# Performance work log

Hardware: AMD Instinct MI355X
Metric: run time of the kernel (lower is better)

The kernel has to match this reference:

```python
import jax, jax.numpy as jnp
import numpy as np

H = 488          # hardcoded grid size in the module
K = 6            # n_targets
ITERS = 10       # n_iterations
RADIUS = 2       # sample_radius (int, used in slicing)
RECLEN = 2 * RADIUS + 1   # avgpool kernel in TorchModalitySampler (upscale=1)
RES = 0.25
THR = 3.0 / RES  # mask threshold on distances


def _greedy_sample(hm):
    """TorchModalitySampler greedy peak extraction for one [H,H] heatmap."""
    aw = H - RECLEN + 1  # avgpool output size (stride 1, valid)

    def step(hm, _):
        # avgpool(kernel=RECLEN, stride=1)
        agg = jax.lax.reduce_window(hm, 0.0, jax.lax.add,
                                    (RECLEN, RECLEN), (1, 1), 'VALID') / (RECLEN * RECLEN)
        flat = jnp.argmax(agg)              # first occurrence of max (row-major)
        r, c = flat // aw, flat % aw
        win = jax.lax.dynamic_slice(hm, (r, c), (RECLEN, RECLEN))
        max_val = win.max()
        # torch.nonzero(hm == max_val)[0] == first row-major match
        fh = jnp.argmax(hm == max_val)
        pt = jnp.stack([fh // H, fh % H]).astype(jnp.float32)
        conf = win.sum()
        hm = jax.lax.dynamic_update_slice(hm, jnp.zeros((RECLEN, RECLEN), hm.dtype), (r, c))
        return hm, (pt, conf)

    _, (pts, confs) = jax.lax.scan(step, hm, None, length=K)
    return pts, confs  # [K,2] float, [K] float


def setup_inputs() -> dict:
    key = jax.random.key(0)
    heatmap = jax.random.uniform(key, (32, 1, H, H), dtype=jnp.float32)
    return {"heatmap": heatmap}


def reference(heatmap):
    B = heatmap.shape[0]
    hm2d = heatmap[:, 0]                       # [B,H,H]
    clusters, _pre_conf = jax.vmap(_greedy_sample)(hm2d)   # [B,K,2]

    ii, jj = jnp.meshgrid(jnp.arange(H), jnp.arange(H), indexing='ij')
    indices = jnp.stack([ii, jj], -1).reshape(-1, 2).astype(jnp.float32)  # [N,2]
    hm_flat = hm2d.reshape(B, -1)              # [B,N]

    def body(_, cl):
        # d: [B,K,N] distances from each cluster to every pixel
        d = jnp.maximum(jnp.linalg.norm(indices[None, None] - cl[:, :, None], axis=-1), 0.001)
        m = d.min(axis=1)                      # [B,N] nearest-cluster distance
        w = (d < THR) * (hm_flat[:, None] / d) * (m[:, None] / d)  # [B,K,N]
        return jnp.einsum('bkn,nd->bkd', w, indices) / w.sum(-1, keepdims=True)

    clusters = jax.lax.fori_loop(0, ITERS, body, clusters)
    new_clusters = jnp.round(clusters).astype(jnp.int32)   # [B,K,2]

    def conf_one(hm, c):
        win = jax.lax.dynamic_slice(hm, (c[0] - RADIUS, c[1] - RADIUS), (2 * RADIUS, 2 * RADIUS))
        return win.sum()

    confidences = jax.vmap(lambda hm, cs: jax.vmap(lambda c: conf_one(hm, c))(cs))(hm2d, new_clusters)
    return new_clusters, confidences
```

## Files before the change

### kernel.cpp

```cpp
#include <hip/hip_runtime.h>

#define H   488
#define HH  (H*H)
#define AW  484
#define KK  6
#define BB  32
#define NB4 (HH/4)

#define SCALE 8388608.0f

#define PHYS(j) ((j) + ((j) >> 5))
#define HPAD 504

__device__ __forceinline__ float mload(const float* h, int i, int j,
                                       const int* rr, const int* rc, int nr) {
    float v = h[i * H + j];
    for (int t = 0; t < nr; ++t)
        if ((unsigned)(i - rr[t]) < 5u && (unsigned)(j - rc[t]) < 5u) v = 0.0f;
    return v;
}

__device__ __forceinline__ unsigned long long mkkey(int s, int c) {
    return ((unsigned long long)(unsigned)s << 32) | (unsigned)~(unsigned)c;
}

__global__ __launch_bounds__(512) void kA(const float* __restrict__ hm,
                                          unsigned long long* __restrict__ blockK) {
    int b  = blockIdx.x & 31;
    int g  = blockIdx.x >> 5;
    int r0 = g * 8;
    int nw = (r0 + 8 <= AW) ? 8 : (AW - r0);
    const float* h = hm + b * HH;
    __shared__ int colsum[8][HPAD];

    int j = threadIdx.x;
    if (j < H) {
        int v[12];
        #pragma unroll
        for (int i = 0; i < 12; ++i) {
            int row = r0 + i;
            v[i] = (row < H) ? (int)(h[row * H + j] * SCALE) : 0;
        }
        int pj = PHYS(j);
        #pragma unroll
        for (int w = 0; w < 8; ++w)
            colsum[w][pj] = v[w] + v[w + 1] + v[w + 2] + v[w + 3] + v[w + 4];
    }
    __syncthreads();

    int wave = threadIdx.x >> 6, lane = threadIdx.x & 63;
    if (wave < nw) {
        int r = r0 + wave;
        int c0 = lane * 8;
        int cs[13];
        #pragma unroll
        for (int t = 0; t < 13; ++t) {
            int idx = c0 + t;
            cs[t] = (idx < H) ? colsum[wave][PHYS(idx)] : 0;
        }
        int s = cs[0] + cs[1] + cs[2] + cs[3] + cs[4];
        unsigned long long best = (c0 < AW) ? mkkey(s, c0) : 0ull;
        #pragma unroll
        for (int t = 1; t < 8; ++t) {
            s += cs[t + 4] - cs[t - 1];
            int c = c0 + t;
            unsigned long long k2 = (c < AW) ? mkkey(s, c) : 0ull;
            if (k2 > best) best = k2;
        }
        #pragma unroll
        for (int off = 4; off; off >>= 1) {
            unsigned long long o = __shfl_down(best, (unsigned)off);
            if (o > best) best = o;
        }
        if ((lane & 7) == 0) {
            int p = lane >> 3;
            blockK[(b * 8 + p) * AW + r] = best;
        }
    }
}

__global__ __launch_bounds__(640) void kB(const float* __restrict__ hm,
                                          const unsigned long long* __restrict__ blockK,
                                          int* __restrict__ rectR, int* __restrict__ rectC,
                                          float* __restrict__ maxv, int* __restrict__ scanres) {
    int b = blockIdx.x;
    const float* h = hm + b * HH;
    __shared__ unsigned long long bK[8 * AW];
    __shared__ unsigned long long rvK[AW];
    __shared__ int rrS[KK], rcS[KK];
    __shared__ int selRs, selCs;
    int tid = threadIdx.x, wave = tid >> 6, lane = tid & 63;

    if (tid < AW) {
        unsigned long long kk[8];
        #pragma unroll
        for (int p = 0; p < 8; ++p) kk[p] = blockK[(b * 8 + p) * AW + tid];
        unsigned long long mk = kk[0];
        #pragma unroll
        for (int p = 1; p < 8; ++p) if (kk[p] > mk) mk = kk[p];
        #pragma unroll
        for (int p = 0; p < 8; ++p) bK[p * AW + tid] = kk[p];
        rvK[tid] = ((mk >> 32) << 20) | ((unsigned long long)(1023 - tid) << 10) | (mk & 0x3FF);
    }
    __syncthreads();

    unsigned long long partK = 0ull;
    int prlo = 0, prhi = -1;

    for (int step = 0; step < KK; ++step) {
        if (wave == 0) {
            unsigned long long win = 0ull;
            if (step == 0) {
                #pragma unroll
                for (int t = 0; t < 8; ++t) {
                    int idx = t * 64 + lane;
                    if (idx < AW) { unsigned long long v = rvK[idx]; if (v > win) win = v; }
                }
                #pragma unroll
                for (int off = 32; off; off >>= 1) {
                    unsigned long long o = __shfl_down(win, (unsigned)off);
                    if (o > win) win = o;
                }
            } else {
                if (lane <= prhi - prlo) win = rvK[prlo + lane];
                if (lane == 9) { if (partK > win) win = partK; }
                #pragma unroll
                for (int off = 8; off; off >>= 1) {
                    unsigned long long o = __shfl_down(win, (unsigned)off);
                    if (o > win) win = o;
                }
            }
            if (lane == 0) {
                int C = 1023 - (int)(win & 0x3FF);
                int R = 1023 - (int)((win >> 10) & 0x3FF);
                rrS[step] = R; rcS[step] = C;
                selRs = R; selCs = C;
            }
        } else if (wave == 1 && step > 0) {
            int m = step - 1;
            int R1 = rrS[m], C1 = rcS[m];
            float wv = -1.0f;
            if (lane < 25) wv = mload(h, R1 + lane / 5, C1 + lane % 5, rrS, rcS, m);
            #pragma unroll
            for (int off = 32; off; off >>= 1) wv = fmaxf(wv, __shfl_down(wv, (unsigned)off));
            if (lane == 0) {
                maxv[b * KK + m]    = wv;
                rectR[b * KK + m]   = R1;
                rectC[b * KK + m]   = C1;
                scanres[b * KK + m] = 0x7fffffff;
            }
        }
        __syncthreads();
        if (step == KK - 1) break;

        int R = selRs, C = selCs;
        int rlo = R > 4 ? R - 4 : 0, rhi = R + 4 < AW ? R + 4 : AW - 1;
        int nr = rhi - rlo + 1;
        if (wave >= 1 && wave <= nr) {
            int r = rlo + (wave - 1);
            int cb0 = (C > 4 ? C - 4 : 0) >> 6;
            int cb1 = ((C + 4 < AW ? C + 4 : AW - 1)) >> 6;
            bool two = (cb1 > cb0);
            int rrL[KK], rcL[KK];
            #pragma unroll
            for (int t = 0; t < KK; ++t) { rrL[t] = rrS[t]; rcL[t] = rcS[t]; }
            int jA0 = cb0 * 64 + lane, jB0 = jA0 + 64;
            int jA1 = cb1 * 64 + lane, jB1 = jA1 + 64;
            float vA0[5], vB0[5], vA1[5], vB1[5];
            #pragma unroll
            for (int i = 0; i < 5; ++i) {
                vA0[i] = (jA0 < H) ? h[(r + i) * H + jA0] : 0.0f;
                vB0[i] = (lane < 4 && jB0 < H) ? h[(r + i) * H + jB0] : 0.0f;
                vA1[i] = (two && jA1 < H) ? h[(r + i) * H + jA1] : 0.0f;
                vB1[i] = (two && lane < 4 && jB1 < H) ? h[(r + i) * H + jB1] : 0.0f;
            }
            #pragma unroll
            for (int t = 0; t < KK; ++t) if (t <= step) {
                int rt = rrL[t], ct = rcL[t];
                #pragma unroll
                for (int i = 0; i < 5; ++i) {
                    if ((unsigned)(r + i - rt) < 5u) {
                        if ((unsigned)(jA0 - ct) < 5u) vA0[i] = 0.0f;
                        if ((unsigned)(jB0 - ct) < 5u) vB0[i] = 0.0f;
                        if ((unsigned)(jA1 - ct) < 5u) vA1[i] = 0.0f;
                        if ((unsigned)(jB1 - ct) < 5u) vB1[i] = 0.0f;
                    }
                }
            }
            int csA0 = 0, csB0 = 0, csA1 = 0, csB1 = 0;
            #pragma unroll
            for (int i = 0; i < 5; ++i) {
                csA0 += (int)(vA0[i] * SCALE); csB0 += (int)(vB0[i] * SCALE);
                csA1 += (int)(vA1[i] * SCALE); csB1 += (int)(vB1[i] * SCALE);
            }
            int s0 = 0, s1 = 0;
            #pragma unroll
            for (int k = 0; k < 5; ++k) {
                int a0 = __shfl_down(csA0, (unsigned)k);
                int a1 = __shfl_down(csA1, (unsigned)k);
                int srcb = lane + k - 64; if (srcb < 0) srcb = 0;
                int b0v = __shfl(csB0, srcb);
                int b1v = __shfl(csB1, srcb);
                s0 += (lane + k < 64) ? a0 : b0v;
                s1 += (lane + k < 64) ? a1 : b1v;
            }
            int c0col = cb0 * 64 + lane, c1col = cb1 * 64 + lane;
            unsigned long long kA_ = (c0col < AW) ? mkkey(s0, c0col) : 0ull;
            unsigned long long kB_ = (two && c1col < AW) ? mkkey(s1, c1col) : 0ull;
            #pragma unroll
            for (int off = 32; off; off >>= 1) {
                unsigned long long oA = __shfl_down(kA_, (unsigned)off);
                unsigned long long oB = __shfl_down(kB_, (unsigned)off);
                if (oA > kA_) kA_ = oA;
                if (oB > kB_) kB_ = oB;
            }
            unsigned long long keyA = __shfl(kA_, 0);
            unsigned long long keyB = __shfl(kB_, 0);
            unsigned long long cand = (lane < 8) ? bK[lane * AW + r] : 0ull;
            if (lane == cb0) cand = keyA;
            if (two && lane == cb1) cand = keyB;
            #pragma unroll
            for (int off = 4; off; off >>= 1) {
                unsigned long long o = __shfl_down(cand, (unsigned)off);
                if (o > cand) cand = o;
            }
            if (lane == 0) {
                rvK[r] = ((cand >> 32) << 20) | ((unsigned long long)(1023 - r) << 10) | (cand & 0x3FF);
                bK[cb0 * AW + r] = keyA;
                if (two) bK[cb1 * AW + r] = keyB;
            }
        } else if (wave == 0) {
            unsigned long long c0 = 0ull;
            #pragma unroll
            for (int t = 0; t < 8; ++t) {
                int idx = t * 64 + lane;
                if (idx < AW && (idx < rlo || idx > rhi)) {
                    unsigned long long v = rvK[idx];
                    if (v > c0) c0 = v;
                }
            }
            #pragma unroll
            for (int off = 32; off; off >>= 1) {
                unsigned long long o = __shfl_down(c0, (unsigned)off);
                if (o > c0) c0 = o;
            }
            partK = __shfl(c0, 0);
            prlo = rlo; prhi = rhi;
        }
        __syncthreads();
    }
    if (wave == 1) {
        int m = KK - 1;
        int R1 = rrS[m], C1 = rcS[m];
        float wv = -1.0f;
        if (lane < 25) wv = mload(h, R1 + lane / 5, C1 + lane % 5, rrS, rcS, m);
        #pragma unroll
        for (int off = 32; off; off >>= 1) wv = fmaxf(wv, __shfl_down(wv, (unsigned)off));
        if (lane == 0) {
            maxv[b * KK + m]    = wv;
            rectR[b * KK + m]   = R1;
            rectC[b * KK + m]   = C1;
            scanres[b * KK + m] = 0x7fffffff;
        }
    }
}

__global__ __launch_bounds__(256) void kC(const float* __restrict__ hm,
                                          const int* __restrict__ rectR, const int* __restrict__ rectC,
                                          const float* __restrict__ maxv, int* __restrict__ scanres) {
    int b     = blockIdx.x & 31;
    int chunk = blockIdx.x >> 5;
    float mv[KK];
    int rr[5], rc[5], lim[KK];
    #pragma unroll
    for (int s = 0; s < KK; ++s) mv[s] = maxv[b * KK + s];
    float minmv = mv[0];
    #pragma unroll
    for (int s = 1; s < KK; ++s) minmv = fminf(minmv, mv[s]);
    #pragma unroll
    for (int t = 0; t < 5; ++t) { rr[t] = rectR[b * KK + t]; rc[t] = rectC[b * KK + t]; }
    int limmax = 0;
    #pragma unroll
    for (int s = 0; s < KK; ++s) {
        lim[s] = (rectR[b * KK + s] + 4) * H + rectC[b * KK + s] + 4;
        limmax = lim[s] > limmax ? lim[s] : limmax;
    }
    const float4* h4 = (const float4*)(hm + b * HH);
    int local[KK];
    #pragma unroll
    for (int s = 0; s < KK; ++s) local[s] = 0x7fffffff;
    for (int i4 = chunk * 256 + threadIdx.x; i4 < NB4; i4 += 8192) {
        if (4 * i4 > limmax) break;
        float4 v = h4[i4];
        float m4 = fmaxf(fmaxf(v.x, v.y), fmaxf(v.z, v.w));
        if (m4 >= minmv) {
            float vs[4] = {v.x, v.y, v.z, v.w};
            #pragma unroll
            for (int e = 0; e < 4; ++e) {
                #pragma unroll
                for (int s = 0; s < KK; ++s) {
                    if (vs[e] == mv[s]) {
                        int n = 4 * i4 + e;
                        if (n <= lim[s]) {
                            int i = n / H, j = n - i * H;
                            bool masked = false;
                            for (int t = 0; t < s; ++t)
                                if ((unsigned)(i - rr[t]) < 5u && (unsigned)(j - rc[t]) < 5u) masked = true;
                            if (!masked && n < local[s]) local[s] = n;
                        }
                    }
                }
            }
        }
    }
    __shared__ int sm[KK];
    if (threadIdx.x < KK) sm[threadIdx.x] = 0x7fffffff;
    __syncthreads();
    #pragma unroll
    for (int s = 0; s < KK; ++s)
        if (local[s] != 0x7fffffff) atomicMin(&sm[s], local[s]);
    __syncthreads();
    if (threadIdx.x < KK && sm[threadIdx.x] != 0x7fffffff)
        atomicMin(&scanres[b * KK + threadIdx.x], sm[threadIdx.x]);
}

__global__ __launch_bounds__(768) void kD(const float* __restrict__ hm,
                                          const int* __restrict__ scanres, float* __restrict__ out) {
    int b = blockIdx.x;
    const float* h = hm + b * HH;
    __shared__ float cly[2][KK], clx[2][KK];
    __shared__ float part[KK][2][3];
    int tid = threadIdx.x;
    if (tid < KK) {
        int fh = scanres[b * KK + tid];
        cly[0][tid] = (float)(fh / H);
        clx[0][tid] = (float)(fh % H);
    }
    __syncthreads();
    int wave = tid >> 6, lane = tid & 63;
    int k = wave >> 1, half = wave & 1;
    int base = half * 64 + lane;

    int di_[4], dj_[4]; bool act_[4];
    #pragma unroll
    for (int s = 0; s < 4; ++s) { act_[s] = false; di_[s] = 0; dj_[s] = 0; }
    {
        int pos = 0;
        #pragma unroll
        for (int r = 0; r < 24; ++r) {
            const int di = r - 11;
            const int u = (di > 0) ? (di - 1) : -di;
            const int vt[12] = {11, 11, 11, 11, 11, 10, 10, 9, 8, 7, 6, 4};
            const int vl = vt[u];
            const int cnt = 2 * vl + 2;
            #pragma unroll
            for (int s = 0; s < 4; ++s) {
                int idx = base + s * 128;
                if (idx >= pos && idx < pos + cnt) {
                    act_[s] = true; di_[s] = di; dj_[s] = -vl + (idx - pos);
                }
            }
            pos += cnt;
        }
    }

    int cur = 0;
    for (int it = 0; it < 10; ++it) {
        float ys[KK], xs[KK];
        #pragma unroll
        for (int q = 0; q < KK; ++q) { ys[q] = cly[cur][q]; xs[q] = clx[cur][q]; }
        float cy = 0.0f, cx = 0.0f;
        #pragma unroll
        for (int q = 0; q < KK; ++q) if (q == k) { cy = ys[q]; cx = xs[q]; }
        int fy = (int)floorf(cy), fx = (int)floorf(cx);
        float sy = 0.0f, sx = 0.0f, sw = 0.0f;
        #pragma unroll
        for (int s = 0; s < 4; ++s) {
            if (act_[s]) {
                int i = fy + di_[s], j = fx + dj_[s];
                if ((unsigned)i < (unsigned)H && (unsigned)j < (unsigned)H) {
                    float hv = h[i * H + j];
                    float fi = (float)i, fj = (float)j;
                    float d2[KK];
                    #pragma unroll
                    for (int q = 0; q < KK; ++q) {
                        float dy = __fsub_rn(fi, ys[q]);
                        float dx = __fsub_rn(fj, xs[q]);
                        d2[q] = __fadd_rn(__fmul_rn(dy, dy), __fmul_rn(dx, dx));
                    }
                    float dyk = __fsub_rn(fi, cy), dxk = __fsub_rn(fj, cx);
                    float d2k = __fadd_rn(__fmul_rn(dyk, dyk), __fmul_rn(dxk, dxk));
                    if (d2k < 144.0f) {
                        float m2 = d2[0];
                        #pragma unroll
                        for (int q = 1; q < KK; ++q) m2 = fminf(m2, d2[q]);
                        float d = fmaxf(__fsqrt_rn(d2k), 0.001f);
                        float m = fmaxf(__fsqrt_rn(m2), 0.001f);
                        float w = __fmul_rn(__fdiv_rn(hv, d), __fdiv_rn(m, d));
                        sw += w;
                        sy += w * fi;
                        sx += w * fj;
                    }
                }
            }
        }
        #pragma unroll
        for (int off = 32; off; off >>= 1) {
            sy += __shfl_down(sy, (unsigned)off);
            sx += __shfl_down(sx, (unsigned)off);
            sw += __shfl_down(sw, (unsigned)off);
        }
        if (lane == 0) { part[k][half][0] = sy; part[k][half][1] = sx; part[k][half][2] = sw; }
        __syncthreads();
        if (tid < KK) {
            float ty = part[tid][0][0] + part[tid][1][0];
            float tx = part[tid][0][1] + part[tid][1][1];
            float tw = part[tid][0][2] + part[tid][1][2];
            cly[cur ^ 1][tid] = ty / tw;
            clx[cur ^ 1][tid] = tx / tw;
        }
        __syncthreads();
        cur ^= 1;
    }
    if (tid < KK) {
        int iy = __float2int_rn(cly[cur][tid]);
        int ix = __float2int_rn(clx[cur][tid]);
        out[b * (KK * 2) + 2 * tid]     = (float)iy;
        out[b * (KK * 2) + 2 * tid + 1] = (float)ix;
        int s0 = iy - 2; if (s0 < 0) s0 = 0; if (s0 > H - 4) s0 = H - 4;
        int s1 = ix - 2; if (s1 < 0) s1 = 0; if (s1 > H - 4) s1 = H - 4;
        double cs = 0.0;
        for (int i = 0; i < 4; ++i)
            for (int j = 0; j < 4; ++j) cs += (double)h[(s0 + i) * H + (s1 + j)];
        out[BB * KK * 2 + b * KK + tid] = (float)cs;
    }
}

extern "C" void kernel_launch(void* const* d_in, const int* in_sizes, int n_in,
                              void* d_out, int out_size, void* d_ws, size_t ws_size,
                              hipStream_t stream) {
    const float* hm = (const float*)d_in[0];
    float* out = (float*)d_out;

    unsigned long long* blockK = (unsigned long long*)d_ws;
    int*    rectR   = (int*)(blockK + BB * 8 * AW);
    int*    rectC   = rectR + BB * KK;
    float*  maxv    = (float*)(rectC + BB * KK);
    int*    scanres = (int*)(maxv + BB * KK);

    kA<<<BB * 61, 512, 0, stream>>>(hm, blockK);
    kB<<<BB, 640, 0, stream>>>(hm, blockK, rectR, rectC, maxv, scanres);
    kC<<<BB * 32, 256, 0, stream>>>(hm, rectR, rectC, maxv, scanres);
    kD<<<BB, 768, 0, stream>>>(hm, scanres, out);
}
```

Baseline: 133.7 us.

## Fuse four kernels into two using in-kernel spin-wait flags between producer and consumer blocks

Merges kA into kB and kC into kD. The consumer blocks (the first 32 block indices) spin on per-batch completion flags written with release stores by the producer blocks. This removes two kernel launches and lets the consumer work for one batch start once its own producers finish, rather than waiting on a full grid boundary. It relies on the producer blocks being scheduled while the consumers spin, which is a deadlock risk. The done flags are never reset, so a later call could see stale MAGIC values unless the workspace is cleared. The scan kernel also changes its chunking, with fewer and larger blocks.

```diff
diff --git a/kernel.cpp b/kernel.cpp
--- a/kernel.cpp
+++ b/kernel.cpp
@@ -6,6 +6,8 @@
 #define KK  6
 #define BB  32
 #define NB4 (HH/4)
+#define NCH 10
+#define MAGIC 0x137F9E24
 
 #define SCALE 8388608.0f
 
@@ -24,73 +26,94 @@
     return ((unsigned long long)(unsigned)s << 32) | (unsigned)~(unsigned)c;
 }
 
-__global__ __launch_bounds__(512) void kA(const float* __restrict__ hm,
-                                          unsigned long long* __restrict__ blockK) {
-    int b  = blockIdx.x & 31;
-    int g  = blockIdx.x >> 5;
-    int r0 = g * 8;
-    int nw = (r0 + 8 <= AW) ? 8 : (AW - r0);
-    const float* h = hm + b * HH;
-    __shared__ int colsum[8][HPAD];
-
-    int j = threadIdx.x;
-    if (j < H) {
-        int v[12];
-        #pragma unroll
-        for (int i = 0; i < 12; ++i) {
-            int row = r0 + i;
-            v[i] = (row < H) ? (int)(h[row * H + j] * SCALE) : 0;
-        }
-        int pj = PHYS(j);
-        #pragma unroll
-        for (int w = 0; w < 8; ++w)
-            colsum[w][pj] = v[w] + v[w + 1] + v[w + 2] + v[w + 3] + v[w + 4];
-    }
-    __syncthreads();
-
-    int wave = threadIdx.x >> 6, lane = threadIdx.x & 63;
-    if (wave < nw) {
-        int r = r0 + wave;
-        int c0 = lane * 8;
-        int cs[13];
-        #pragma unroll
-        for (int t = 0; t < 13; ++t) {
-            int idx = c0 + t;
-            cs[t] = (idx < H) ? colsum[wave][PHYS(idx)] : 0;
-        }
-        int s = cs[0] + cs[1] + cs[2] + cs[3] + cs[4];
-        unsigned long long best = (c0 < AW) ? mkkey(s, c0) : 0ull;
-        #pragma unroll
-        for (int t = 1; t < 8; ++t) {
-            s += cs[t + 4] - cs[t - 1];
-            int c = c0 + t;
-            unsigned long long k2 = (c < AW) ? mkkey(s, c) : 0ull;
-            if (k2 > best) best = k2;
-        }
-        #pragma unroll
-        for (int off = 4; off; off >>= 1) {
-            unsigned long long o = __shfl_down(best, (unsigned)off);
-            if (o > best) best = o;
-        }
-        if ((lane & 7) == 0) {
-            int p = lane >> 3;
-            blockK[(b * 8 + p) * AW + r] = best;
-        }
-    }
-}
-
-__global__ __launch_bounds__(640) void kB(const float* __restrict__ hm,
-                                          const unsigned long long* __restrict__ blockK,
-                                          int* __restrict__ rectR, int* __restrict__ rectC,
-                                          float* __restrict__ maxv, int* __restrict__ scanres) {
-    int b = blockIdx.x;
-    const float* h = hm + b * HH;
-    __shared__ unsigned long long bK[8 * AW];
-    __shared__ unsigned long long rvK[AW];
+union Sm1 {
+    int colsum[8][HPAD];
+    struct { unsigned long long bK[8 * AW]; unsigned long long rvK[AW]; } kb;
+};
+
+__global__ __launch_bounds__(640, 8) void k1(const float* __restrict__ hm,
+                                             unsigned long long* __restrict__ blockK,
+                                             int* __restrict__ rectR, int* __restrict__ rectC,
+                                             float* __restrict__ maxv, int* __restrict__ scanres,
+                                             int* __restrict__ doneA) {
+    __shared__ Sm1 sm;
     __shared__ int rrS[KK], rcS[KK];
     __shared__ int selRs, selCs;
     int tid = threadIdx.x, wave = tid >> 6, lane = tid & 63;
 
+    if (blockIdx.x >= 32) {
+        int idx = blockIdx.x - 32;
+        int b  = idx & 31;
+        int g  = idx >> 5;
+        int r0 = g * 8;
+        int nw = (r0 + 8 <= AW) ? 8 : (AW - r0);
+        const float* h = hm + b * HH;
+
+        int j = tid;
+        if (j < H) {
+            int v[12];
+            #pragma unroll
+            for (int i = 0; i < 12; ++i) {
+                int row = r0 + i;
+                v[i] = (row < H) ? (int)(h[row * H + j] * SCALE) : 0;
+            }
+            int pj = PHYS(j);
+            #pragma unroll
+            for (int w = 0; w < 8; ++w)
+                sm.colsum[w][pj] = v[w] + v[w + 1] + v[w + 2] + v[w + 3] + v[w + 4];
+        }
+        __syncthreads();
+
+        if (wave < nw) {
+            int r = r0 + wave;
+            int c0 = lane * 8;
+            int cs[13];
+            #pragma unroll
+            for (int t = 0; t < 13; ++t) {
+                int ix = c0 + t;
+                cs[t] = (ix < H) ? sm.colsum[wave][PHYS(ix)] : 0;
+            }
+            int s = cs[0] + cs[1] + cs[2] + cs[3] + cs[4];
+            unsigned long long best = (c0 < AW) ? mkkey(s, c0) : 0ull;
+            #pragma unroll
+            for (int t = 1; t < 8; ++t) {
+                s += cs[t + 4] - cs[t - 1];
+                int c = c0 + t;
+                unsigned long long k2v = (c < AW) ? mkkey(s, c) : 0ull;
+                if (k2v > best) best = k2v;
+            }
+            #pragma unroll
+            for (int off = 4; off; off >>= 1) {
+                unsigned long long o = __shfl_down(best, (unsigned)off);
+                if (o > best) best = o;
+            }
+            if ((lane & 7) == 0) {
+                int p = lane >> 3;
+                blockK[(b * 8 + p) * AW + r] = best;
+            }
+        }
+        __syncthreads();
+        if (tid == 0)
+            __hip_atomic_store(&doneA[b * 61 + g], MAGIC, __ATOMIC_RELEASE, __HIP_MEMORY_SCOPE_AGENT);
+        return;
+    }
+
+    int b = blockIdx.x;
+    const float* h = hm + b * HH;
+
+    if (wave == 0) {
+        bool done = false;
+        do {
+            int v = (lane < 61)
+                ? __hip_atomic_load(&doneA[b * 61 + lane], __ATOMIC_RELAXED, __HIP_MEMORY_SCOPE_AGENT)
+                : MAGIC;
+            done = __all(v == MAGIC);
+            if (!done) __builtin_amdgcn_s_sleep(8);
+        } while (!done);
+        __threadfence();
+    }
+    __syncthreads();
+
     if (tid < AW) {
         unsigned long long kk[8];
         #pragma unroll
@@ -99,8 +122,8 @@
         #pragma unroll
         for (int p = 1; p < 8; ++p) if (kk[p] > mk) mk = kk[p];
         #pragma unroll
-        for (int p = 0; p < 8; ++p) bK[p * AW + tid] = kk[p];
-        rvK[tid] = ((mk >> 32) << 20) | ((unsigned long long)(1023 - tid) << 10) | (mk & 0x3FF);
+        for (int p = 0; p < 8; ++p) sm.kb.bK[p * AW + tid] = kk[p];
+        sm.kb.rvK[tid] = ((mk >> 32) << 20) | ((unsigned long long)(1023 - tid) << 10) | (mk & 0x3FF);
     }
     __syncthreads();
 
@@ -114,7 +137,7 @@
                 #pragma unroll
                 for (int t = 0; t < 8; ++t) {
                     int idx = t * 64 + lane;
-                    if (idx < AW) { unsigned long long v = rvK[idx]; if (v > win) win = v; }
+                    if (idx < AW) { unsigned long long v = sm.kb.rvK[idx]; if (v > win) win = v; }
                 }
                 #pragma unroll
                 for (int off = 32; off; off >>= 1) {
@@ -122,7 +145,7 @@
                     if (o > win) win = o;
                 }
             } else {
-                if (lane <= prhi - prlo) win = rvK[prlo + lane];
+                if (lane <= prhi - prlo) win = sm.kb.rvK[prlo + lane];
                 if (lane == 9) { if (partK > win) win = partK; }
                 #pragma unroll
                 for (int off = 8; off; off >>= 1) {
@@ -216,7 +239,7 @@
             }
             unsigned long long keyA = __shfl(kA_, 0);
             unsigned long long keyB = __shfl(kB_, 0);
-            unsigned long long cand = (lane < 8) ? bK[lane * AW + r] : 0ull;
+            unsigned long long cand = (lane < 8) ? sm.kb.bK[lane * AW + r] : 0ull;
             if (lane == cb0) cand = keyA;
             if (two && lane == cb1) cand = keyB;
             #pragma unroll
@@ -225,9 +248,9 @@
                 if (o > cand) cand = o;
             }
             if (lane == 0) {
-                rvK[r] = ((cand >> 32) << 20) | ((unsigned long long)(1023 - r) << 10) | (cand & 0x3FF);
-                bK[cb0 * AW + r] = keyA;
-                if (two) bK[cb1 * AW + r] = keyB;
+                sm.kb.rvK[r] = ((cand >> 32) << 20) | ((unsigned long long)(1023 - r) << 10) | (cand & 0x3FF);
+                sm.kb.bK[cb0 * AW + r] = keyA;
+                if (two) sm.kb.bK[cb1 * AW + r] = keyB;
             }
         } else if (wave == 0) {
             unsigned long long c0 = 0ull;
@@ -235,7 +258,7 @@
             for (int t = 0; t < 8; ++t) {
                 int idx = t * 64 + lane;
                 if (idx < AW && (idx < rlo || idx > rhi)) {
-                    unsigned long long v = rvK[idx];
+                    unsigned long long v = sm.kb.rvK[idx];
                     if (v > c0) c0 = v;
                 }
             }
@@ -265,79 +288,98 @@
     }
 }
 
-__global__ __launch_bounds__(256) void kC(const float* __restrict__ hm,
-                                          const int* __restrict__ rectR, const int* __restrict__ rectC,
-                                          const float* __restrict__ maxv, int* __restrict__ scanres) {
-    int b     = blockIdx.x & 31;
-    int chunk = blockIdx.x >> 5;
-    float mv[KK];
-    int rr[5], rc[5], lim[KK];
-    #pragma unroll
-    for (int s = 0; s < KK; ++s) mv[s] = maxv[b * KK + s];
-    float minmv = mv[0];
-    #pragma unroll
-    for (int s = 1; s < KK; ++s) minmv = fminf(minmv, mv[s]);
-    #pragma unroll
-    for (int t = 0; t < 5; ++t) { rr[t] = rectR[b * KK + t]; rc[t] = rectC[b * KK + t]; }
-    int limmax = 0;
-    #pragma unroll
-    for (int s = 0; s < KK; ++s) {
-        lim[s] = (rectR[b * KK + s] + 4) * H + rectC[b * KK + s] + 4;
-        limmax = lim[s] > limmax ? lim[s] : limmax;
-    }
-    const float4* h4 = (const float4*)(hm + b * HH);
-    int local[KK];
-    #pragma unroll
-    for (int s = 0; s < KK; ++s) local[s] = 0x7fffffff;
-    for (int i4 = chunk * 256 + threadIdx.x; i4 < NB4; i4 += 8192) {
-        if (4 * i4 > limmax) break;
-        float4 v = h4[i4];
-        float m4 = fmaxf(fmaxf(v.x, v.y), fmaxf(v.z, v.w));
-        if (m4 >= minmv) {
-            float vs[4] = {v.x, v.y, v.z, v.w};
-            #pragma unroll
-            for (int e = 0; e < 4; ++e) {
+__global__ __launch_bounds__(768, 8) void k2(const float* __restrict__ hm,
+                                             const int* __restrict__ rectR, const int* __restrict__ rectC,
+                                             const float* __restrict__ maxv, int* __restrict__ scanres,
+                                             int* __restrict__ doneC, float* __restrict__ out) {
+    int tid = threadIdx.x, wave = tid >> 6, lane = tid & 63;
+
+    if (blockIdx.x >= 32) {
+        int idx   = blockIdx.x - 32;
+        int b     = idx & 31;
+        int chunk = idx >> 5;
+        float mv[KK];
+        int rr[5], rc[5], lim[KK];
+        #pragma unroll
+        for (int s = 0; s < KK; ++s) mv[s] = maxv[b * KK + s];
+        float minmv = mv[0];
+        #pragma unroll
+        for (int s = 1; s < KK; ++s) minmv = fminf(minmv, mv[s]);
+        #pragma unroll
+        for (int t = 0; t < 5; ++t) { rr[t] = rectR[b * KK + t]; rc[t] = rectC[b * KK + t]; }
+        int limmax = 0;
+        #pragma unroll
+        for (int s = 0; s < KK; ++s) {
+            lim[s] = (rectR[b * KK + s] + 4) * H + rectC[b * KK + s] + 4;
+            limmax = lim[s] > limmax ? lim[s] : limmax;
+        }
+        const float4* h4 = (const float4*)(hm + b * HH);
+        int local[KK];
+        #pragma unroll
+        for (int s = 0; s < KK; ++s) local[s] = 0x7fffffff;
+        for (int i4 = chunk * 768 + tid; i4 < NB4; i4 += 768 * NCH) {
+            if (4 * i4 > limmax) break;
+            float4 v = h4[i4];
+            float m4 = fmaxf(fmaxf(v.x, v.y), fmaxf(v.z, v.w));
+            if (m4 >= minmv) {
+                float vs[4] = {v.x, v.y, v.z, v.w};
                 #pragma unroll
-                for (int s = 0; s < KK; ++s) {
-                    if (vs[e] == mv[s]) {
-                        int n = 4 * i4 + e;
-                        if (n <= lim[s]) {
-                            int i = n / H, j = n - i * H;
-                            bool masked = false;
-                            for (int t = 0; t < s; ++t)
-                                if ((unsigned)(i - rr[t]) < 5u && (unsigned)(j - rc[t]) < 5u) masked = true;
-                            if (!masked && n < local[s]) local[s] = n;
+                for (int e = 0; e < 4; ++e) {
+                    #pragma unroll
+                    for (int s = 0; s < KK; ++s) {
+                        if (vs[e] == mv[s]) {
+                            int n = 4 * i4 + e;
+                            if (n <= lim[s]) {
+                                int i = n / H, j = n - i * H;
+                                bool masked = false;
+                                for (int t = 0; t < s; ++t)
+                                    if ((unsigned)(i - rr[t]) < 5u && (unsigned)(j - rc[t]) < 5u) masked = true;
+                                if (!masked && n < local[s]) local[s] = n;
+                            }
                         }
                     }
                 }
             }
         }
-    }
-    __shared__ int sm[KK];
-    if (threadIdx.x < KK) sm[threadIdx.x] = 0x7fffffff;
-    __syncthreads();
-    #pragma unroll
-    for (int s = 0; s < KK; ++s)
-        if (local[s] != 0x7fffffff) atomicMin(&sm[s], local[s]);
-    __syncthreads();
-    if (threadIdx.x < KK && sm[threadIdx.x] != 0x7fffffff)
-        atomicMin(&scanres[b * KK + threadIdx.x], sm[threadIdx.x]);
-}
-
-__global__ __launch_bounds__(768) void kD(const float* __restrict__ hm,
-                                          const int* __restrict__ scanres, float* __restrict__ out) {
+        __shared__ int smC[KK];
+        if (tid < KK) smC[tid] = 0x7fffffff;
+        __syncthreads();
+        #pragma unroll
+        for (int s = 0; s < KK; ++s)
+            if (local[s] != 0x7fffffff) atomicMin(&smC[s], local[s]);
+        __syncthreads();
+        if (tid < KK && smC[tid] != 0x7fffffff)
+            atomicMin(&scanres[b * KK + tid], smC[tid]);
+        __syncthreads();
+        if (tid == 0)
+            __hip_atomic_store(&doneC[b * NCH + chunk], MAGIC, __ATOMIC_RELEASE, __HIP_MEMORY_SCOPE_AGENT);
+        return;
+    }
+
     int b = blockIdx.x;
     const float* h = hm + b * HH;
     __shared__ float cly[2][KK], clx[2][KK];
     __shared__ float part[KK][2][3];
-    int tid = threadIdx.x;
+
+    if (wave == 0) {
+        bool done = false;
+        do {
+            int v = (lane < NCH)
+                ? __hip_atomic_load(&doneC[b * NCH + lane], __ATOMIC_RELAXED, __HIP_MEMORY_SCOPE_AGENT)
+                : MAGIC;
+            done = __all(v == MAGIC);
+            if (!done) __builtin_amdgcn_s_sleep(8);
+        } while (!done);
+        __threadfence();
+    }
+    __syncthreads();
+
     if (tid < KK) {
-        int fh = scanres[b * KK + tid];
+        int fh = __hip_atomic_load(&scanres[b * KK + tid], __ATOMIC_RELAXED, __HIP_MEMORY_SCOPE_AGENT);
         cly[0][tid] = (float)(fh / H);
         clx[0][tid] = (float)(fh % H);
     }
     __syncthreads();
-    int wave = tid >> 6, lane = tid & 63;
     int k = wave >> 1, half = wave & 1;
     int base = half * 64 + lane;
 
@@ -447,9 +489,9 @@
     int*    rectC   = rectR + BB * KK;
     float*  maxv    = (float*)(rectC + BB * KK);
     int*    scanres = (int*)(maxv + BB * KK);
-
-    kA<<<BB * 61, 512, 0, stream>>>(hm, blockK);
-    kB<<<BB, 640, 0, stream>>>(hm, blockK, rectR, rectC, maxv, scanres);
-    kC<<<BB * 32, 256, 0, stream>>>(hm, rectR, rectC, maxv, scanres);
-    kD<<<BB, 768, 0, stream>>>(hm, scanres, out);
+    int*    doneA   = scanres + BB * KK;
+    int*    doneC   = doneA + BB * 61;
+
+    k1<<<32 + BB * 61, 640, 0, stream>>>(hm, blockK, rectR, rectC, maxv, scanres, doneA);
+    k2<<<32 + BB * NCH, 768, 0, stream>>>(hm, rectR, rectC, maxv, scanres, doneC, out);
 }
```

Result: slower. 187.6 us (+40.3%).

## Fuse greedy selection, first-match scan and mean-shift kernels into one block per batch

Applied to the files above, without the earlier changes.

Merges kernels kB, kC and kD into one 1024-thread kernel per batch image. Intermediate rectangles, max values and scan results stay in shared memory instead of going through global workspace, and two kernel launches go away. In exchange, the first-match scan, which used to spread over 32 blocks per image, now runs on a single 1024-thread block per image bounded by limmax. That reduces parallelism across CUs to only 32 blocks total.

```diff
diff --git a/kernel.cpp b/kernel.cpp
--- a/kernel.cpp
+++ b/kernel.cpp
@@ -79,16 +79,19 @@
     }
 }
 
-__global__ __launch_bounds__(640) void kB(const float* __restrict__ hm,
-                                          const unsigned long long* __restrict__ blockK,
-                                          int* __restrict__ rectR, int* __restrict__ rectC,
-                                          float* __restrict__ maxv, int* __restrict__ scanres) {
+__global__ __launch_bounds__(1024) void kBCD(const float* __restrict__ hm,
+                                             const unsigned long long* __restrict__ blockK,
+                                             float* __restrict__ out) {
     int b = blockIdx.x;
     const float* h = hm + b * HH;
     __shared__ unsigned long long bK[8 * AW];
     __shared__ unsigned long long rvK[AW];
     __shared__ int rrS[KK], rcS[KK];
+    __shared__ float wvS[KK];
     __shared__ int selRs, selCs;
+    __shared__ int smC[KK];
+    __shared__ float cly[2][KK], clx[2][KK];
+    __shared__ float part[KK][2][3];
     int tid = threadIdx.x, wave = tid >> 6, lane = tid & 63;
 
     if (tid < AW) {
@@ -143,12 +146,7 @@
             if (lane < 25) wv = mload(h, R1 + lane / 5, C1 + lane % 5, rrS, rcS, m);
             #pragma unroll
             for (int off = 32; off; off >>= 1) wv = fmaxf(wv, __shfl_down(wv, (unsigned)off));
-            if (lane == 0) {
-                maxv[b * KK + m]    = wv;
-                rectR[b * KK + m]   = R1;
-                rectC[b * KK + m]   = C1;
-                scanres[b * KK + m] = 0x7fffffff;
-            }
+            if (lane == 0) wvS[m] = wv;
         }
         __syncthreads();
         if (step == KK - 1) break;
@@ -256,41 +254,32 @@
         if (lane < 25) wv = mload(h, R1 + lane / 5, C1 + lane % 5, rrS, rcS, m);
         #pragma unroll
         for (int off = 32; off; off >>= 1) wv = fmaxf(wv, __shfl_down(wv, (unsigned)off));
-        if (lane == 0) {
-            maxv[b * KK + m]    = wv;
-            rectR[b * KK + m]   = R1;
-            rectC[b * KK + m]   = C1;
-            scanres[b * KK + m] = 0x7fffffff;
-        }
-    }
-}
-
-__global__ __launch_bounds__(256) void kC(const float* __restrict__ hm,
-                                          const int* __restrict__ rectR, const int* __restrict__ rectC,
-                                          const float* __restrict__ maxv, int* __restrict__ scanres) {
-    int b     = blockIdx.x & 31;
-    int chunk = blockIdx.x >> 5;
-    float mv[KK];
-    int rr[5], rc[5], lim[KK];
-    #pragma unroll
-    for (int s = 0; s < KK; ++s) mv[s] = maxv[b * KK + s];
+        if (lane == 0) wvS[m] = wv;
+    }
+    __syncthreads();
+
+    if (tid < KK) smC[tid] = 0x7fffffff;
+    float mv[KK]; int rr[5], rc[5], lim[KK];
+    #pragma unroll
+    for (int s = 0; s < KK; ++s) mv[s] = wvS[s];
     float minmv = mv[0];
     #pragma unroll
     for (int s = 1; s < KK; ++s) minmv = fminf(minmv, mv[s]);
     #pragma unroll
-    for (int t = 0; t < 5; ++t) { rr[t] = rectR[b * KK + t]; rc[t] = rectC[b * KK + t]; }
+    for (int t = 0; t < 5; ++t) { rr[t] = rrS[t]; rc[t] = rcS[t]; }
     int limmax = 0;
     #pragma unroll
     for (int s = 0; s < KK; ++s) {
-        lim[s] = (rectR[b * KK + s] + 4) * H + rectC[b * KK + s] + 4;
+        lim[s] = (rrS[s] + 4) * H + rcS[s] + 4;
         limmax = lim[s] > limmax ? lim[s] : limmax;
     }
-    const float4* h4 = (const float4*)(hm + b * HH);
+    int ub = (limmax >> 2) + 1; if (ub > NB4) ub = NB4;
+    const float4* h4 = (const float4*)h;
     int local[KK];
     #pragma unroll
     for (int s = 0; s < KK; ++s) local[s] = 0x7fffffff;
-    for (int i4 = chunk * 256 + threadIdx.x; i4 < NB4; i4 += 8192) {
-        if (4 * i4 > limmax) break;
+    __syncthreads();
+    for (int i4 = tid; i4 < ub; i4 += 1024) {
         float4 v = h4[i4];
         float m4 = fmaxf(fmaxf(v.x, v.y), fmaxf(v.z, v.w));
         if (m4 >= minmv) {
@@ -313,31 +302,17 @@
             }
         }
     }
-    __shared__ int sm[KK];
-    if (threadIdx.x < KK) sm[threadIdx.x] = 0x7fffffff;
-    __syncthreads();
     #pragma unroll
     for (int s = 0; s < KK; ++s)
-        if (local[s] != 0x7fffffff) atomicMin(&sm[s], local[s]);
-    __syncthreads();
-    if (threadIdx.x < KK && sm[threadIdx.x] != 0x7fffffff)
-        atomicMin(&scanres[b * KK + threadIdx.x], sm[threadIdx.x]);
-}
-
-__global__ __launch_bounds__(768) void kD(const float* __restrict__ hm,
-                                          const int* __restrict__ scanres, float* __restrict__ out) {
-    int b = blockIdx.x;
-    const float* h = hm + b * HH;
-    __shared__ float cly[2][KK], clx[2][KK];
-    __shared__ float part[KK][2][3];
-    int tid = threadIdx.x;
+        if (local[s] != 0x7fffffff) atomicMin(&smC[s], local[s]);
+    __syncthreads();
+
     if (tid < KK) {
-        int fh = scanres[b * KK + tid];
+        int fh = smC[tid];
         cly[0][tid] = (float)(fh / H);
         clx[0][tid] = (float)(fh % H);
     }
     __syncthreads();
-    int wave = tid >> 6, lane = tid & 63;
     int k = wave >> 1, half = wave & 1;
     int base = half * 64 + lane;
 
@@ -366,51 +341,53 @@
 
     int cur = 0;
     for (int it = 0; it < 10; ++it) {
-        float ys[KK], xs[KK];
-        #pragma unroll
-        for (int q = 0; q < KK; ++q) { ys[q] = cly[cur][q]; xs[q] = clx[cur][q]; }
-        float cy = 0.0f, cx = 0.0f;
-        #pragma unroll
-        for (int q = 0; q < KK; ++q) if (q == k) { cy = ys[q]; cx = xs[q]; }
-        int fy = (int)floorf(cy), fx = (int)floorf(cx);
         float sy = 0.0f, sx = 0.0f, sw = 0.0f;
-        #pragma unroll
-        for (int s = 0; s < 4; ++s) {
-            if (act_[s]) {
-                int i = fy + di_[s], j = fx + dj_[s];
-                if ((unsigned)i < (unsigned)H && (unsigned)j < (unsigned)H) {
-                    float hv = h[i * H + j];
-                    float fi = (float)i, fj = (float)j;
-                    float d2[KK];
-                    #pragma unroll
-                    for (int q = 0; q < KK; ++q) {
-                        float dy = __fsub_rn(fi, ys[q]);
-                        float dx = __fsub_rn(fj, xs[q]);
-                        d2[q] = __fadd_rn(__fmul_rn(dy, dy), __fmul_rn(dx, dx));
+        if (k < KK) {
+            float ys[KK], xs[KK];
+            #pragma unroll
+            for (int q = 0; q < KK; ++q) { ys[q] = cly[cur][q]; xs[q] = clx[cur][q]; }
+            float cy = 0.0f, cx = 0.0f;
+            #pragma unroll
+            for (int q = 0; q < KK; ++q) if (q == k) { cy = ys[q]; cx = xs[q]; }
+            int fy = (int)floorf(cy), fx = (int)floorf(cx);
+            #pragma unroll
+            for (int s = 0; s < 4; ++s) {
+                if (act_[s]) {
+                    int i = fy + di_[s], j = fx + dj_[s];
+                    if ((unsigned)i < (unsigned)H && (unsigned)j < (unsigned)H) {
+                        float hv = h[i * H + j];
+                        float fi = (float)i, fj = (float)j;
+                        float d2[KK];
+                        #pragma unroll
+                        for (int q = 0; q < KK; ++q) {
+                            float dy = __fsub_rn(fi, ys[q]);
+                            float dx = __fsub_rn(fj, xs[q]);
+                            d2[q] = __fadd_rn(__fmul_rn(dy, dy), __fmul_rn(dx, dx));
+                        }
+                        float dyk = __fsub_rn(fi, cy), dxk = __fsub_rn(fj, cx);
+                        float d2k = __fadd_rn(__fmul_rn(dyk, dyk), __fmul_rn(dxk, dxk));
+                        if (d2k < 144.0f) {
+                            float m2 = d2[0];
+                            #pragma unroll
+                            for (int q = 1; q < KK; ++q) m2 = fminf(m2, d2[q]);
+                            float d = fmaxf(__fsqrt_rn(d2k), 0.001f);
+                            float m = fmaxf(__fsqrt_rn(m2), 0.001f);
+                            float w = __fmul_rn(__fdiv_rn(hv, d), __fdiv_rn(m, d));
+                            sw += w;
+                            sy += w * fi;
+                            sx += w * fj;
+                        }
                     }
-                    float dyk = __fsub_rn(fi, cy), dxk = __fsub_rn(fj, cx);
-                    float d2k = __fadd_rn(__fmul_rn(dyk, dyk), __fmul_rn(dxk, dxk));
-                    if (d2k < 144.0f) {
-                        float m2 = d2[0];
-                        #pragma unroll
-                        for (int q = 1; q < KK; ++q) m2 = fminf(m2, d2[q]);
-                        float d = fmaxf(__fsqrt_rn(d2k), 0.001f);
-                        float m = fmaxf(__fsqrt_rn(m2), 0.001f);
-                        float w = __fmul_rn(__fdiv_rn(hv, d), __fdiv_rn(m, d));
-                        sw += w;
-                        sy += w * fi;
-                        sx += w * fj;
-                    }
-                }
-            }
-        }
-        #pragma unroll
-        for (int off = 32; off; off >>= 1) {
-            sy += __shfl_down(sy, (unsigned)off);
-            sx += __shfl_down(sx, (unsigned)off);
-            sw += __shfl_down(sw, (unsigned)off);
-        }
-        if (lane == 0) { part[k][half][0] = sy; part[k][half][1] = sx; part[k][half][2] = sw; }
+                }
+            }
+            #pragma unroll
+            for (int off = 32; off; off >>= 1) {
+                sy += __shfl_down(sy, (unsigned)off);
+                sx += __shfl_down(sx, (unsigned)off);
+                sw += __shfl_down(sw, (unsigned)off);
+            }
+            if (lane == 0) { part[k][half][0] = sy; part[k][half][1] = sx; part[k][half][2] = sw; }
+        }
         __syncthreads();
         if (tid < KK) {
             float ty = part[tid][0][0] + part[tid][1][0];
@@ -443,13 +420,7 @@
     float* out = (float*)d_out;
 
     unsigned long long* blockK = (unsigned long long*)d_ws;
-    int*    rectR   = (int*)(blockK + BB * 8 * AW);
-    int*    rectC   = rectR + BB * KK;
-    float*  maxv    = (float*)(rectC + BB * KK);
-    int*    scanres = (int*)(maxv + BB * KK);
 
     kA<<<BB * 61, 512, 0, stream>>>(hm, blockK);
-    kB<<<BB, 640, 0, stream>>>(hm, blockK, rectR, rectC, maxv, scanres);
-    kC<<<BB * 32, 256, 0, stream>>>(hm, rectR, rectC, maxv, scanres);
-    kD<<<BB, 768, 0, stream>>>(hm, scanres, out);
+    kBCD<<<BB, 1024, 0, stream>>>(hm, blockK, out);
 }
```

Result: slower. 181.8 us (+36.0%).

## Fuse scan and refinement kernels using last-block-done atomic counter

Applied to the files above, without the earlier changes.

Merges the first-match scan kernel and the mean-shift refinement kernel into one launch. Each batch gets NCH=10 blocks of 768 threads instead of 32 blocks of 256, and a per-batch atomic counter, reset in kB, lets the last finishing block run the refinement. That block reads scanres through an atomic so it sees the other blocks' results. This saves one kernel launch and its gap, at the cost of less scan parallelism and a serialized tail in one block per batch.

```diff
diff --git a/kernel.cpp b/kernel.cpp
--- a/kernel.cpp
+++ b/kernel.cpp
@@ -6,6 +6,7 @@
 #define KK  6
 #define BB  32
 #define NB4 (HH/4)
+#define NCH 10
 
 #define SCALE 8388608.0f
 
@@ -82,7 +83,8 @@
 __global__ __launch_bounds__(640) void kB(const float* __restrict__ hm,
                                           const unsigned long long* __restrict__ blockK,
                                           int* __restrict__ rectR, int* __restrict__ rectC,
-                                          float* __restrict__ maxv, int* __restrict__ scanres) {
+                                          float* __restrict__ maxv, int* __restrict__ scanres,
+                                          int* __restrict__ cntC) {
     int b = blockIdx.x;
     const float* h = hm + b * HH;
     __shared__ unsigned long long bK[8 * AW];
@@ -90,6 +92,8 @@
     __shared__ int rrS[KK], rcS[KK];
     __shared__ int selRs, selCs;
     int tid = threadIdx.x, wave = tid >> 6, lane = tid & 63;
+
+    if (tid == 639) cntC[b] = 0;
 
     if (tid < AW) {
         unsigned long long kk[8];
@@ -265,79 +269,84 @@
     }
 }
 
-__global__ __launch_bounds__(256) void kC(const float* __restrict__ hm,
-                                          const int* __restrict__ rectR, const int* __restrict__ rectC,
-                                          const float* __restrict__ maxv, int* __restrict__ scanres) {
+__global__ __launch_bounds__(768) void kCD(const float* __restrict__ hm,
+                                           const int* __restrict__ rectR, const int* __restrict__ rectC,
+                                           const float* __restrict__ maxv, int* __restrict__ scanres,
+                                           int* __restrict__ cntC, float* __restrict__ out) {
     int b     = blockIdx.x & 31;
     int chunk = blockIdx.x >> 5;
-    float mv[KK];
-    int rr[5], rc[5], lim[KK];
-    #pragma unroll
-    for (int s = 0; s < KK; ++s) mv[s] = maxv[b * KK + s];
-    float minmv = mv[0];
-    #pragma unroll
-    for (int s = 1; s < KK; ++s) minmv = fminf(minmv, mv[s]);
-    #pragma unroll
-    for (int t = 0; t < 5; ++t) { rr[t] = rectR[b * KK + t]; rc[t] = rectC[b * KK + t]; }
-    int limmax = 0;
-    #pragma unroll
-    for (int s = 0; s < KK; ++s) {
-        lim[s] = (rectR[b * KK + s] + 4) * H + rectC[b * KK + s] + 4;
-        limmax = lim[s] > limmax ? lim[s] : limmax;
-    }
-    const float4* h4 = (const float4*)(hm + b * HH);
-    int local[KK];
-    #pragma unroll
-    for (int s = 0; s < KK; ++s) local[s] = 0x7fffffff;
-    for (int i4 = chunk * 256 + threadIdx.x; i4 < NB4; i4 += 8192) {
-        if (4 * i4 > limmax) break;
-        float4 v = h4[i4];
-        float m4 = fmaxf(fmaxf(v.x, v.y), fmaxf(v.z, v.w));
-        if (m4 >= minmv) {
-            float vs[4] = {v.x, v.y, v.z, v.w};
-            #pragma unroll
-            for (int e = 0; e < 4; ++e) {
+    int tid = threadIdx.x, wave = tid >> 6, lane = tid & 63;
+    const float* h = hm + b * HH;
+
+    {
+        float mv[KK];
+        int rr[5], rc[5], lim[KK];
+        #pragma unroll
+        for (int s = 0; s < KK; ++s) mv[s] = maxv[b * KK + s];
+        float minmv = mv[0];
+        #pragma unroll
+        for (int s = 1; s < KK; ++s) minmv = fminf(minmv, mv[s]);
+        #pragma unroll
+        for (int t = 0; t < 5; ++t) { rr[t] = rectR[b * KK + t]; rc[t] = rectC[b * KK + t]; }
+        int limmax = 0;
+        #pragma unroll
+        for (int s = 0; s < KK; ++s) {
+            lim[s] = (rectR[b * KK + s] + 4) * H + rectC[b * KK + s] + 4;
+            limmax = lim[s] > limmax ? lim[s] : limmax;
+        }
+        const float4* h4 = (const float4*)h;
+        int local[KK];
+        #pragma unroll
+        for (int s = 0; s < KK; ++s) local[s] = 0x7fffffff;
+        for (int i4 = chunk * 768 + tid; i4 < NB4; i4 += 768 * NCH) {
+            if (4 * i4 > limmax) break;
+            float4 v = h4[i4];
+            float m4 = fmaxf(fmaxf(v.x, v.y), fmaxf(v.z, v.w));
+            if (m4 >= minmv) {
+                float vs[4] = {v.x, v.y, v.z, v.w};
                 #pragma unroll
-                for (int s = 0; s < KK; ++s) {
-                    if (vs[e] == mv[s]) {
-                        int n = 4 * i4 + e;
-                        if (n <= lim[s]) {
-                            int i = n / H, j = n - i * H;
-                            bool masked = false;
-                            for (int t = 0; t < s; ++t)
-                                if ((unsigned)(i - rr[t]) < 5u && (unsigned)(j - rc[t]) < 5u) masked = true;
-                            if (!masked && n < local[s]) local[s] = n;
+                for (int e = 0; e < 4; ++e) {
+                    #pragma unroll
+                    for (int s = 0; s < KK; ++s) {
+                        if (vs[e] == mv[s]) {
+                            int n = 4 * i4 + e;
+                            if (n <= lim[s]) {
+                                int i = n / H, j = n - i * H;
+                                bool masked = false;
+                                for (int t = 0; t < s; ++t)
+                                    if ((unsigned)(i - rr[t]) < 5u && (unsigned)(j - rc[t]) < 5u) masked = true;
+                                if (!masked && n < local[s]) local[s] = n;
+                            }
                         }
                     }
                 }
             }
         }
-    }
-    __shared__ int sm[KK];
-    if (threadIdx.x < KK) sm[threadIdx.x] = 0x7fffffff;
+        __shared__ int smC[KK];
+        if (tid < KK) smC[tid] = 0x7fffffff;
+        __syncthreads();
+        #pragma unroll
+        for (int s = 0; s < KK; ++s)
+            if (local[s] != 0x7fffffff) atomicMin(&smC[s], local[s]);
+        __syncthreads();
+        if (tid < KK && smC[tid] != 0x7fffffff)
+            atomicMin(&scanres[b * KK + tid], smC[tid]);
+    }
     __syncthreads();
-    #pragma unroll
-    for (int s = 0; s < KK; ++s)
-        if (local[s] != 0x7fffffff) atomicMin(&sm[s], local[s]);
+
+    __shared__ int sh_old;
+    if (tid == 0) sh_old = atomicAdd(&cntC[b], 1);
     __syncthreads();
-    if (threadIdx.x < KK && sm[threadIdx.x] != 0x7fffffff)
-        atomicMin(&scanres[b * KK + threadIdx.x], sm[threadIdx.x]);
-}
-
-__global__ __launch_bounds__(768) void kD(const float* __restrict__ hm,
-                                          const int* __restrict__ scanres, float* __restrict__ out) {
-    int b = blockIdx.x;
-    const float* h = hm + b * HH;
+    if (sh_old != NCH - 1) return;
+
     __shared__ float cly[2][KK], clx[2][KK];
     __shared__ float part[KK][2][3];
-    int tid = threadIdx.x;
     if (tid < KK) {
-        int fh = scanres[b * KK + tid];
+        int fh = atomicMin(&scanres[b * KK + tid], 0x7fffffff);
         cly[0][tid] = (float)(fh / H);
         clx[0][tid] = (float)(fh % H);
     }
     __syncthreads();
-    int wave = tid >> 6, lane = tid & 63;
     int k = wave >> 1, half = wave & 1;
     int base = half * 64 + lane;
 
@@ -447,9 +456,9 @@
     int*    rectC   = rectR + BB * KK;
     float*  maxv    = (float*)(rectC + BB * KK);
     int*    scanres = (int*)(maxv + BB * KK);
+    int*    cntC    = scanres + BB * KK;
 
     kA<<<BB * 61, 512, 0, stream>>>(hm, blockK);
-    kB<<<BB, 640, 0, stream>>>(hm, blockK, rectR, rectC, maxv, scanres);
-    kC<<<BB * 32, 256, 0, stream>>>(hm, rectR, rectC, maxv, scanres);
-    kD<<<BB, 768, 0, stream>>>(hm, scanres, out);
-}
+    kB<<<BB, 640, 0, stream>>>(hm, blockK, rectR, rectC, maxv, scanres, cntC);
+    kCD<<<BB * NCH, 768, 0, stream>>>(hm, rectR, rectC, maxv, scanres, cntC, out);
+}
```

Result: no change. 131.6 us, median of 2 (-1.5%).
